# Performance work log

Measured on AMD Instinct MI355X. Metric: run time of the kernel, lower is better.

The kernel has to match this reference:

```python
import jax, jax.numpy as jnp
import numpy as np

EMBED_DIM = 256
N_LEVELS = 4
N_HEADS = 8
N_POINTS = 4
HEAD_DIM = EMBED_DIM // N_HEADS
N_QUERIES = 8192
BATCH = 2
LEVEL_SHAPES = np.array([[128, 128], [64, 64], [32, 32], [16, 16]], dtype=np.int32)
HMAX, WMAX = 128, 128
EPS = 1e-5


def setup_inputs() -> dict:
    key = jax.random.key(0)
    ks = jax.random.split(key, 10)
    scale = 1.0 / np.sqrt(EMBED_DIM)
    query = jax.random.normal(ks[0], (N_QUERIES, EMBED_DIM), jnp.float32)
    xy_reference_points = jax.random.uniform(ks[1], (N_QUERIES, 2), jnp.float32, 0.05, 0.95)
    val = jax.random.normal(ks[2], (BATCH, HMAX, WMAX, N_LEVELS, EMBED_DIM), jnp.float32)
    # zero outside each level's valid support (mimics sparse COO: absent entries read as 0)
    hh = jnp.arange(HMAX)[:, None, None]
    ww = jnp.arange(WMAX)[None, :, None]
    lh = jnp.asarray(LEVEL_SHAPES[:, 0])[None, None, :]
    lw = jnp.asarray(LEVEL_SHAPES[:, 1])[None, None, :]
    mask = ((hh < lh) & (ww < lw)).astype(jnp.float32)
    stacked_value_tensors = val * mask[None, :, :, :, None]
    return {
        "query": query,
        "xy_reference_points": xy_reference_points,
        "stacked_value_tensors": stacked_value_tensors,
        "W_off": (jax.random.normal(ks[3], (EMBED_DIM, N_LEVELS * N_POINTS * N_HEADS * 2)) * scale * 0.1).astype(jnp.float32),
        "b_off": (jax.random.normal(ks[4], (N_LEVELS * N_POINTS * N_HEADS * 2,)) * 0.5).astype(jnp.float32),
        "W_attn": (jax.random.normal(ks[5], (EMBED_DIM, N_LEVELS * N_POINTS * N_HEADS)) * scale).astype(jnp.float32),
        "b_attn": jnp.zeros((N_LEVELS * N_POINTS * N_HEADS,), jnp.float32),
        "W_out": (jax.random.normal(ks[6], (EMBED_DIM, EMBED_DIM)) * scale).astype(jnp.float32),
        "b_out": jnp.zeros((EMBED_DIM,), jnp.float32),
        "batch_offsets": jnp.array([0, N_QUERIES // 2], jnp.int32),
        "spatial_shapes": jnp.asarray(LEVEL_SHAPES, jnp.int32),
    }


def reference(query, xy_reference_points, stacked_value_tensors, W_off, b_off,
              W_attn, b_attn, W_out, b_out, batch_offsets, spatial_shapes):
    Q = query.shape[0]
    # sampling offsets & attention weights (torch Linear with W stored [in,out])
    off = (query @ W_off + b_off).reshape(Q, N_LEVELS, N_POINTS, N_HEADS, 2)
    aw = (query @ W_attn + b_attn).reshape(Q, N_LEVELS * N_POINTS, N_HEADS)
    aw = jax.nn.softmax(aw, axis=1).reshape(Q, N_LEVELS, N_POINTS, N_HEADS)
    # sampling locations: sigmoid(inverse_sigmoid(ref) + offsets), then map (0,1)->(-1,1)
    r = jnp.clip(xy_reference_points, 0.0, 1.0)
    inv = jnp.log(jnp.clip(r, EPS, 1.0) / jnp.clip(1.0 - r, EPS, 1.0))
    loc = jax.nn.sigmoid(inv[:, None, None, None, :] + off) * 2.0 - 1.0  # (Q,L,P,H,2)
    # per-query batch index from batch_offsets (start index per batch element)
    bidx = jnp.searchsorted(batch_offsets, jnp.arange(Q), side="right") - 1  # (Q,)
    b = bidx[:, None, None, None]
    h_sz = spatial_shapes[:, 0].astype(loc.dtype)[None, :, None, None]
    w_sz = spatial_shapes[:, 1].astype(loc.dtype)[None, :, None, None]
    x = ((loc[..., 0] + 1.0) * w_sz - 1.0) / 2.0  # (Q,L,P,H)
    y = ((loc[..., 1] + 1.0) * h_sz - 1.0) / 2.0
    x0 = jnp.floor(x).astype(jnp.int32); x1 = x0 + 1
    y0 = jnp.floor(y).astype(jnp.int32); y1 = y0 + 1
    wcap = (spatial_shapes[:, 1] - 1).astype(jnp.int32)[None, :, None, None]
    hcap = (spatial_shapes[:, 0] - 1).astype(jnp.int32)[None, :, None, None]
    x0 = jnp.clip(x0, 0, wcap); x1 = jnp.clip(x1, 0, wcap)
    y0 = jnp.clip(y0, 0, hcap); y1 = jnp.clip(y1, 0, hcap)
    x0f = x0.astype(x.dtype); x1f = x1.astype(x.dtype)
    y0f = y0.astype(y.dtype); y1f = y1.astype(y.dtype)
    wa = (x1f - x) * (y1f - y)  # pairs with (x0,y0), as in source
    wb = (x1f - x) * (y - y0f)  # (x0,y1)
    wc = (x - x0f) * (y1f - y)  # (x1,y0)
    wd = (x - x0f) * (y - y0f)  # (x1,y1)
    V = stacked_value_tensors.reshape(BATCH, HMAX, WMAX, N_LEVELS, N_HEADS, HEAD_DIM)
    l = jnp.arange(N_LEVELS)[None, :, None, None]
    h = jnp.arange(N_HEADS)[None, None, None, :]
    # NOTE: source indexes (batch, x, y, level, head) -> x indexes the height dim; levels are square
    def g(xi, yi):
        return V[b, xi, yi, l, h]  # (Q,L,P,H,HEAD_DIM)
    sampled = (wa[..., None] * g(x0, y0) + wb[..., None] * g(x0, y1)
               + wc[..., None] * g(x1, y0) + wd[..., None] * g(x1, y1))
    out = jnp.einsum("qlphd,qlph->qhd", sampled, aw).reshape(Q, EMBED_DIM)
    return out @ W_out + b_out
```

## Files before the change

kernel.cpp:

```cpp
#include <hip/hip_runtime.h>
#include <math.h>

#define ED      256
#define NL      4
#define NH      8
#define NP      4
#define HD      32
#define HMAX    128
#define WMAX    128
#define NLP     16
#define NC      128
#define NOFF_AW 384
#define QPB     4
#define NBK     1024
#define BSTRIDE (HMAX*WMAX*NL*ED)
#define XSTRIDE (WMAX*NL*ED)
#define YSTRIDE (NL*ED)
#define RPB     21760
#define PBC     (RPB*256)

typedef __attribute__((ext_vector_type(8))) __fp16   f16x8;
typedef __attribute__((ext_vector_type(4))) __fp16   f16x4;
typedef __attribute__((ext_vector_type(4))) float    f32x4;

__constant__ int LBASE_ROW[4] = {0, 16384, 20480, 21504};

__global__ __launch_bounds__(1024) void msda_prep_kernel(
    const float* __restrict__ V,
    const float* __restrict__ W_off,
    const float* __restrict__ W_attn,
    const float* __restrict__ W_out,
    const float* __restrict__ refp,
    const int*   __restrict__ batch_off,
    int n_batch,
    __fp16* __restrict__ Vc,
    __fp16* __restrict__ WcatT,
    __fp16* __restrict__ WoutT,
    int* __restrict__ bucket_of,
    int* __restrict__ perm,
    int nq, int nb, int nCompact, int nWconv)
{
    __shared__ int cnt[NBK];
    __shared__ int scan[NBK];
    const int bid = blockIdx.x;
    const int t   = threadIdx.x;

    if (bid < nCompact) {
        const int r    = bid * 16 + (t >> 6);
        const int lane = t & 63;
        const int e    = lane << 2;
        const int total_rows = nb * RPB;
        if (r < total_rows) {
            const int b  = r / RPB;
            const int rr = r - b * RPB;
            int l, base;
            if (rr < 16384)      { l = 0; base = 0; }
            else if (rr < 20480) { l = 1; base = 16384; }
            else if (rr < 21504) { l = 2; base = 20480; }
            else                 { l = 3; base = 21504; }
            const int pos = rr - base;
            const int lsh = 7 - l;
            const int xi  = pos >> lsh;
            const int yi  = pos & ((1 << lsh) - 1);
            const float4 src = *(const float4*)&V[(size_t)b * BSTRIDE +
                (size_t)xi * XSTRIDE + (size_t)yi * YSTRIDE + l * ED + e];
            f16x4 d;
            d[0] = (__fp16)src.x; d[1] = (__fp16)src.y;
            d[2] = (__fp16)src.z; d[3] = (__fp16)src.w;
            *(f16x4*)&Vc[(size_t)r * 256 + e] = d;
        }
    } else if (bid < nCompact + nWconv) {
        const int idx = (bid - nCompact) * 1024 + t;
        const int t2 = NOFF_AW * ED;
        const int t3 = ED * ED;
        if (idx < t2) {
            int c = idx >> 8, e = idx & 255;
            float v = (c < ED) ? W_off[e * ED + c] : W_attn[e * NC + (c - ED)];
            WcatT[idx] = (__fp16)v;
        } else if (idx < t2 + t3) {
            int i = idx - t2;
            int c = i >> 8, e = i & 255;
            WoutT[i] = (__fp16)W_out[e * ED + c];
        }
    } else {
        cnt[t] = 0;
        __syncthreads();
        const int iters = (nq + 1023) >> 10;
        for (int i = 0; i < iters; ++i) {
            int q = i * 1024 + t;
            if (q < nq) {
                int b = 0;
                for (int j = 1; j < n_batch; ++j)
                    if (batch_off[j] <= q) b = j;
                b = min(b, 3);
                float rx = refp[q * 2 + 0], ry = refp[q * 2 + 1];
                int bx = min(15, max(0, (int)(rx * 16.f)));
                int by = min(15, max(0, (int)(ry * 16.f)));
                int bk = (b << 8) | (by << 4) | bx;
                bucket_of[q] = bk;
                atomicAdd(&cnt[bk], 1);
            }
        }
        __syncthreads();
        scan[t] = cnt[t];
        __syncthreads();
        for (int d = 1; d < NBK; d <<= 1) {
            int v = scan[t];
            int u = (t >= d) ? scan[t - d] : 0;
            __syncthreads();
            scan[t] = v + u;
            __syncthreads();
        }
        cnt[t] = scan[t] - cnt[t];
        __syncthreads();
        for (int i = 0; i < iters; ++i) {
            int q = i * 1024 + t;
            if (q < nq) {
                int bk = bucket_of[q];
                int pos = atomicAdd(&cnt[bk], 1);
                perm[pos] = q;
            }
        }
    }
}

__global__ __launch_bounds__(256) void gemm_f16_kernel(
    const float*  __restrict__ A,
    const __fp16* __restrict__ BT,
    const float* __restrict__ bias0,
    const float* __restrict__ bias1,
    float* __restrict__ C,
    int M, int NTOT, int bias_split)
{
    const int wave = threadIdx.x >> 6;
    const int lane = threadIdx.x & 63;
    const int gw   = blockIdx.x * 4 + wave;
    const int ngroups = NTOT >> 6;
    const int mg = gw / ngroups, ng = gw % ngroups;
    const int m16 = mg * 16, n64 = ng * 64;
    if (m16 >= M) return;

    const int mrow = lane & 15;
    const int quad = lane >> 4;

    const float4* Arow = (const float4*)(A + (size_t)(m16 + mrow) * 256 + quad * 8);
    const f16x8* B0 = (const f16x8*)(BT + (size_t)(n64 +  0 + mrow) * 256 + quad * 8);
    const f16x8* B1 = (const f16x8*)(BT + (size_t)(n64 + 16 + mrow) * 256 + quad * 8);
    const f16x8* B2 = (const f16x8*)(BT + (size_t)(n64 + 32 + mrow) * 256 + quad * 8);
    const f16x8* B3 = (const f16x8*)(BT + (size_t)(n64 + 48 + mrow) * 256 + quad * 8);

    f32x4 acc0 = {0.f,0.f,0.f,0.f}, acc1 = acc0, acc2 = acc0, acc3 = acc0;
    #pragma unroll
    for (int kb = 0; kb < 8; ++kb) {
        float4 a0 = Arow[kb * 8 + 0];
        float4 a1 = Arow[kb * 8 + 1];
        float av[8] = {a0.x, a0.y, a0.z, a0.w, a1.x, a1.y, a1.z, a1.w};
        f16x8 ah, al;
        #pragma unroll
        for (int j = 0; j < 8; ++j) {
            __fp16 h = (__fp16)av[j];
            ah[j] = h;
            al[j] = (__fp16)(av[j] - (float)h);
        }
        f16x8 b0 = B0[kb * 4], b1 = B1[kb * 4], b2 = B2[kb * 4], b3 = B3[kb * 4];
        acc0 = __builtin_amdgcn_mfma_f32_16x16x32_f16(ah, b0, acc0, 0, 0, 0);
        acc1 = __builtin_amdgcn_mfma_f32_16x16x32_f16(ah, b1, acc1, 0, 0, 0);
        acc2 = __builtin_amdgcn_mfma_f32_16x16x32_f16(ah, b2, acc2, 0, 0, 0);
        acc3 = __builtin_amdgcn_mfma_f32_16x16x32_f16(ah, b3, acc3, 0, 0, 0);
        acc0 = __builtin_amdgcn_mfma_f32_16x16x32_f16(al, b0, acc0, 0, 0, 0);
        acc1 = __builtin_amdgcn_mfma_f32_16x16x32_f16(al, b1, acc1, 0, 0, 0);
        acc2 = __builtin_amdgcn_mfma_f32_16x16x32_f16(al, b2, acc2, 0, 0, 0);
        acc3 = __builtin_amdgcn_mfma_f32_16x16x32_f16(al, b3, acc3, 0, 0, 0);
    }

    const int col = lane & 15;
    f32x4 accs[4] = {acc0, acc1, acc2, acc3};
    #pragma unroll
    for (int i = 0; i < 4; ++i) {
        int n = n64 + i * 16 + col;
        float b = (n < bias_split) ? bias0[n] : bias1[n - bias_split];
        #pragma unroll
        for (int r = 0; r < 4; ++r) {
            int row = m16 + quad * 4 + r;
            C[(size_t)row * NTOT + n] = accs[i][r] + b;
        }
    }
}

__global__ __launch_bounds__(256) void gemm_ff16_kernel(
    const __fp16* __restrict__ A,
    const __fp16* __restrict__ BT,
    const float* __restrict__ bias,
    float* __restrict__ C,
    int M, int NTOT)
{
    const int wave = threadIdx.x >> 6;
    const int lane = threadIdx.x & 63;
    const int gw   = blockIdx.x * 4 + wave;
    const int ngroups = NTOT >> 6;
    const int mg = gw / ngroups, ng = gw % ngroups;
    const int m16 = mg * 16, n64 = ng * 64;
    if (m16 >= M) return;

    const int mrow = lane & 15;
    const int quad = lane >> 4;

    const f16x8* Arow = (const f16x8*)(A + (size_t)(m16 + mrow) * 256 + quad * 8);
    const f16x8* B0 = (const f16x8*)(BT + (size_t)(n64 +  0 + mrow) * 256 + quad * 8);
    const f16x8* B1 = (const f16x8*)(BT + (size_t)(n64 + 16 + mrow) * 256 + quad * 8);
    const f16x8* B2 = (const f16x8*)(BT + (size_t)(n64 + 32 + mrow) * 256 + quad * 8);
    const f16x8* B3 = (const f16x8*)(BT + (size_t)(n64 + 48 + mrow) * 256 + quad * 8);

    f32x4 acc0 = {0.f,0.f,0.f,0.f}, acc1 = acc0, acc2 = acc0, acc3 = acc0;
    #pragma unroll
    for (int kb = 0; kb < 8; ++kb) {
        f16x8 af = Arow[kb * 4];
        acc0 = __builtin_amdgcn_mfma_f32_16x16x32_f16(af, B0[kb * 4], acc0, 0, 0, 0);
        acc1 = __builtin_amdgcn_mfma_f32_16x16x32_f16(af, B1[kb * 4], acc1, 0, 0, 0);
        acc2 = __builtin_amdgcn_mfma_f32_16x16x32_f16(af, B2[kb * 4], acc2, 0, 0, 0);
        acc3 = __builtin_amdgcn_mfma_f32_16x16x32_f16(af, B3[kb * 4], acc3, 0, 0, 0);
    }

    const int col = lane & 15;
    f32x4 accs[4] = {acc0, acc1, acc2, acc3};
    #pragma unroll
    for (int i = 0; i < 4; ++i) {
        int n = n64 + i * 16 + col;
        float b = bias[n];
        #pragma unroll
        for (int r = 0; r < 4; ++r) {
            int row = m16 + quad * 4 + r;
            C[(size_t)row * NTOT + n] = accs[i][r] + b;
        }
    }
}

__global__ __launch_bounds__(256) void msda_sample_kernel(
    const float*  __restrict__ refp,
    const __fp16* __restrict__ Vc,
    const float*  __restrict__ off_aw,
    const int*    __restrict__ perm,
    const int*    __restrict__ batch_off,
    int n_batch,
    __fp16* __restrict__ out_pre,
    int q_total)
{
    __shared__ int    sqid[QPB];
    __shared__ float  law[QPB][NC];
    __shared__ float2 sminv[QPB][NH];
    __shared__ float2 sref[QPB];
    __shared__ int4   soff[QPB][NC];
    __shared__ float4 swt[QPB][NC];

    const int t = threadIdx.x;
    const int chunk = gridDim.x >> 3;
    const int pblk  = (blockIdx.x & 7) * chunk + (blockIdx.x >> 3);
    const int q0 = pblk * QPB;

    if (t < QPB) sqid[t] = perm[q0 + t];
    __syncthreads();

    {
        const int s = t >> 6, c = t & 63;
        const float* row = off_aw + (size_t)sqid[s] * NOFF_AW + ED;
        law[s][c]      = row[c];
        law[s][c + 64] = row[c + 64];
    }
    __syncthreads();

    if (t < QPB * NH) {
        const int s = t >> 3, h = t & 7;
        float m = -1e30f;
        #pragma unroll
        for (int lp = 0; lp < NLP; ++lp) m = fmaxf(m, law[s][lp * NH + h]);
        float sum = 0.f;
        #pragma unroll
        for (int lp = 0; lp < NLP; ++lp) sum += __expf(law[s][lp * NH + h] - m);
        sminv[s][h] = make_float2(m, 1.f / sum);
    } else if (t < QPB * NH + QPB) {
        const int s = t - QPB * NH;
        const int qid = sqid[s];
        float rx = refp[qid * 2 + 0], ry = refp[qid * 2 + 1];
        rx = fminf(fmaxf(rx, 0.f), 1.f);
        ry = fminf(fmaxf(ry, 0.f), 1.f);
        float ivx = __logf(fmaxf(rx, 1e-5f) / fmaxf(1.f - rx, 1e-5f));
        float ivy = __logf(fmaxf(ry, 1e-5f) / fmaxf(1.f - ry, 1e-5f));
        sref[s] = make_float2(ivx, ivy);
    }
    __syncthreads();

    {
        const int s = t >> 6;
        const int qid = sqid[s];
        int b = 0;
        for (int i = 1; i < n_batch; ++i)
            if (batch_off[i] <= qid) b = i;
        const int cb = b * PBC;
        const float2 iv = sref[s];
        const float* offrow = off_aw + (size_t)qid * NOFF_AW;

        #pragma unroll
        for (int half = 0; half < 2; ++half) {
            const int c = (t & 63) + half * 64;
            const int l = c >> 5;
            const int h = c & 7;
            const int lsh = 7 - l;
            const int sz  = 1 << lsh;
            const int cap = sz - 1;

            const float2 mi = sminv[s][h];
            const float a = __expf(law[s][c] - mi.x) * mi.y;

            const float ox = offrow[c * 2 + 0], oy = offrow[c * 2 + 1];
            float lx = 2.f / (1.f + __expf(-(iv.x + ox))) - 1.f;
            float ly = 2.f / (1.f + __expf(-(iv.y + oy))) - 1.f;
            float x = ((lx + 1.f) * (float)sz - 1.f) * 0.5f;
            float y = ((ly + 1.f) * (float)sz - 1.f) * 0.5f;
            int x0 = (int)floorf(x), y0 = (int)floorf(y);
            int x1 = x0 + 1, y1 = y0 + 1;
            x0 = min(max(x0, 0), cap); x1 = min(max(x1, 0), cap);
            y0 = min(max(y0, 0), cap); y1 = min(max(y1, 0), cap);
            float x0f = (float)x0, x1f = (float)x1;
            float y0f = (float)y0, y1f = (float)y1;

            float4 w;
            w.x = a * (x1f - x) * (y1f - y);
            w.y = a * (x1f - x) * (y - y0f);
            w.z = a * (x - x0f) * (y1f - y);
            w.w = a * (x - x0f) * (y - y0f);
            swt[s][c] = w;
            const int lb = cb + (LBASE_ROW[l] << 8);
            int4 o;
            o.x = lb + (((x0 << lsh) + y0) << 8);
            o.y = lb + (((x0 << lsh) + y1) << 8);
            o.z = lb + (((x1 << lsh) + y0) << 8);
            o.w = lb + (((x1 << lsh) + y1) << 8);
            soff[s][c] = o;
        }
    }
    __syncthreads();

    {
        const int s    = t >> 6;
        const int lane = t & 63;
        const int h    = lane >> 3;
        const int d4   = (lane & 7) << 2;
        const int inner = h * HD + d4;
        float4 acc = {0.f, 0.f, 0.f, 0.f};
        #pragma unroll 4
        for (int lp = 0; lp < NLP; ++lp) {
            const int c = lp * NH + h;
            int4   o = soff[s][c];
            float4 w = swt[s][c];
            f16x4 v0 = *(const f16x4*)&Vc[o.x + inner];
            f16x4 v1 = *(const f16x4*)&Vc[o.y + inner];
            f16x4 v2 = *(const f16x4*)&Vc[o.z + inner];
            f16x4 v3 = *(const f16x4*)&Vc[o.w + inner];
            acc.x += w.x*(float)v0[0] + w.y*(float)v1[0] + w.z*(float)v2[0] + w.w*(float)v3[0];
            acc.y += w.x*(float)v0[1] + w.y*(float)v1[1] + w.z*(float)v2[1] + w.w*(float)v3[1];
            acc.z += w.x*(float)v0[2] + w.y*(float)v1[2] + w.z*(float)v2[2] + w.w*(float)v3[2];
            acc.w += w.x*(float)v0[3] + w.y*(float)v1[3] + w.z*(float)v2[3] + w.w*(float)v3[3];
        }
        f16x4 o4;
        o4[0] = (__fp16)acc.x; o4[1] = (__fp16)acc.y;
        o4[2] = (__fp16)acc.z; o4[3] = (__fp16)acc.w;
        *(f16x4*)&out_pre[(size_t)sqid[s] * ED + inner] = o4;
    }
}

extern "C" void kernel_launch(void* const* d_in, const int* in_sizes, int n_in,
                              void* d_out, int out_size, void* d_ws, size_t ws_size,
                              hipStream_t stream) {
    const float* query  = (const float*)d_in[0];
    const float* refp   = (const float*)d_in[1];
    const float* V      = (const float*)d_in[2];
    const float* W_off  = (const float*)d_in[3];
    const float* b_off  = (const float*)d_in[4];
    const float* W_attn = (const float*)d_in[5];
    const float* b_attn = (const float*)d_in[6];
    const float* W_out  = (const float*)d_in[7];
    const float* b_out  = (const float*)d_in[8];
    const int*   boff   = (const int*)d_in[9];
    const int*   spat   = (const int*)d_in[10];
    const int n_batch   = in_sizes[9];
    const int nq        = in_sizes[0] / ED;
    const int nb        = in_sizes[2] / BSTRIDE;
    float* out = (float*)d_out;

    char* ws = (char*)d_ws;
    float*   off_aw    = (float*)ws;
    int*     perm      = (int*)(off_aw + (size_t)nq * NOFF_AW);
    int*     bucket_of = perm + nq;
    __fp16*  WcatT     = (__fp16*)(bucket_of + nq);
    __fp16*  WoutT     = WcatT + NOFF_AW * ED;
    __fp16*  out_pre   = WoutT + ED * ED;
    __fp16*  Vc        = out_pre + (size_t)nq * ED;

    {
        int nCompact = (nb * RPB + 15) / 16;
        int nWconv   = (NOFF_AW * ED + ED * ED + 1023) / 1024;
        msda_prep_kernel<<<nCompact + nWconv + 1, 1024, 0, stream>>>(
            V, W_off, W_attn, W_out, refp, boff, n_batch,
            Vc, WcatT, WoutT, bucket_of, perm, nq, nb, nCompact, nWconv);
    }
    {
        int waves = (nq / 16) * (NOFF_AW / 64);
        gemm_f16_kernel<<<(waves + 3) / 4, 256, 0, stream>>>(
            query, WcatT, b_off, b_attn, off_aw, nq, NOFF_AW, ED);
    }
    {
        msda_sample_kernel<<<nq / QPB, 256, 0, stream>>>(
            refp, Vc, off_aw, perm, boff, n_batch, out_pre, nq);
    }
    {
        int waves = (nq / 16) * (ED / 64);
        gemm_ff16_kernel<<<(waves + 3) / 4, 256, 0, stream>>>(
            out_pre, WoutT, b_out, out, nq, ED);
    }
}
```

Measured before the change: 266.4 us.

## Replace per-query gather with tile-binned sampling through shared-memory patches

Drops the query bucket sort. A plan kernel now computes bilinear weights per sample and scatters compact records into per-tile bins of each level using block-local histograms and global cursors. A tile kernel loads a 9x9 value patch into LDS and serves all samples in that tile from it, and a reduce kernel then sums the per-level-point samples into out_pre. This aims to turn scattered global gathers into LDS reuse. The cost is two extra launches, a large record buffer and an intermediate sampled buffer round-trip, fp16-packed weights, and a slow overflow fallback path.

```diff
diff --git a/kernel.cpp b/kernel.cpp
--- a/kernel.cpp
+++ b/kernel.cpp
@@ -12,36 +12,37 @@
 #define NC      128
 #define NOFF_AW 384
 #define QPB     4
-#define NBK     1024
 #define BSTRIDE (HMAX*WMAX*NL*ED)
 #define XSTRIDE (WMAX*NL*ED)
 #define YSTRIDE (NL*ED)
 #define RPB     21760
-#define PBC     (RPB*256)
+#define TILES_PB 340
+#define RECPB   2097152
+#define MAXB    4
 
 typedef __attribute__((ext_vector_type(8))) __fp16   f16x8;
 typedef __attribute__((ext_vector_type(4))) __fp16   f16x4;
 typedef __attribute__((ext_vector_type(4))) float    f32x4;
 
 __constant__ int LBASE_ROW[4] = {0, 16384, 20480, 21504};
+__constant__ int TBASE[4]     = {0, 256, 320, 336};
+
+__device__ __forceinline__ unsigned pack2h(float a, float b) {
+    union { __fp16 h[2]; unsigned u; } u;
+    u.h[0] = (__fp16)a; u.h[1] = (__fp16)b; return u.u;
+}
 
 __global__ __launch_bounds__(1024) void msda_prep_kernel(
     const float* __restrict__ V,
     const float* __restrict__ W_off,
     const float* __restrict__ W_attn,
     const float* __restrict__ W_out,
-    const float* __restrict__ refp,
-    const int*   __restrict__ batch_off,
-    int n_batch,
     __fp16* __restrict__ Vc,
     __fp16* __restrict__ WcatT,
     __fp16* __restrict__ WoutT,
-    int* __restrict__ bucket_of,
-    int* __restrict__ perm,
-    int nq, int nb, int nCompact, int nWconv)
-{
-    __shared__ int cnt[NBK];
-    __shared__ int scan[NBK];
+    unsigned* __restrict__ cursor,
+    int nb, int nCompact, int nWconv)
+{
     const int bid = blockIdx.x;
     const int t   = threadIdx.x;
 
@@ -83,44 +84,7 @@
             WoutT[i] = (__fp16)W_out[e * ED + c];
         }
     } else {
-        cnt[t] = 0;
-        __syncthreads();
-        const int iters = (nq + 1023) >> 10;
-        for (int i = 0; i < iters; ++i) {
-            int q = i * 1024 + t;
-            if (q < nq) {
-                int b = 0;
-                for (int j = 1; j < n_batch; ++j)
-                    if (batch_off[j] <= q) b = j;
-                b = min(b, 3);
-                float rx = refp[q * 2 + 0], ry = refp[q * 2 + 1];
-                int bx = min(15, max(0, (int)(rx * 16.f)));
-                int by = min(15, max(0, (int)(ry * 16.f)));
-                int bk = (b << 8) | (by << 4) | bx;
-                bucket_of[q] = bk;
-                atomicAdd(&cnt[bk], 1);
-            }
-        }
-        __syncthreads();
-        scan[t] = cnt[t];
-        __syncthreads();
-        for (int d = 1; d < NBK; d <<= 1) {
-            int v = scan[t];
-            int u = (t >= d) ? scan[t - d] : 0;
-            __syncthreads();
-            scan[t] = v + u;
-            __syncthreads();
-        }
-        cnt[t] = scan[t] - cnt[t];
-        __syncthreads();
-        for (int i = 0; i < iters; ++i) {
-            int q = i * 1024 + t;
-            if (q < nq) {
-                int bk = bucket_of[q];
-                int pos = atomicAdd(&cnt[bk], 1);
-                perm[pos] = q;
-            }
-        }
+        for (int i = t; i < TILES_PB * nb; i += 1024) cursor[i] = 0u;
     }
 }
 
@@ -235,34 +199,31 @@
     }
 }
 
-__global__ __launch_bounds__(256) void msda_sample_kernel(
+__global__ __launch_bounds__(256) void msda_plan_kernel(
     const float*  __restrict__ refp,
     const __fp16* __restrict__ Vc,
     const float*  __restrict__ off_aw,
-    const int*    __restrict__ perm,
     const int*    __restrict__ batch_off,
-    int n_batch,
-    __fp16* __restrict__ out_pre,
-    int q_total)
-{
-    __shared__ int    sqid[QPB];
-    __shared__ float  law[QPB][NC];
-    __shared__ float2 sminv[QPB][NH];
-    __shared__ float2 sref[QPB];
-    __shared__ int4   soff[QPB][NC];
-    __shared__ float4 swt[QPB][NC];
-
-    const int t = threadIdx.x;
-    const int chunk = gridDim.x >> 3;
-    const int pblk  = (blockIdx.x & 7) * chunk + (blockIdx.x >> 3);
-    const int q0 = pblk * QPB;
-
-    if (t < QPB) sqid[t] = perm[q0 + t];
-    __syncthreads();
+    int n_batch, int nb,
+    unsigned* __restrict__ cursor,
+    int4*     __restrict__ recB,
+    __fp16*   __restrict__ sampled,
+    int nq)
+{
+    __shared__ float    law[QPB][NC];
+    __shared__ float2   sminv[QPB][NH];
+    __shared__ float2   sref[QPB];
+    __shared__ unsigned hist[TILES_PB * MAXB];
+
+    const int t  = threadIdx.x;
+    const int q0 = blockIdx.x * QPB;
+    const int tiles_total = TILES_PB * nb;
+
+    for (int i = t; i < TILES_PB * MAXB; i += 256) hist[i] = 0u;
 
     {
         const int s = t >> 6, c = t & 63;
-        const float* row = off_aw + (size_t)sqid[s] * NOFF_AW + ED;
+        const float* row = off_aw + (size_t)(q0 + s) * NOFF_AW + ED;
         law[s][c]      = row[c];
         law[s][c + 64] = row[c + 64];
     }
@@ -279,7 +240,7 @@
         sminv[s][h] = make_float2(m, 1.f / sum);
     } else if (t < QPB * NH + QPB) {
         const int s = t - QPB * NH;
-        const int qid = sqid[s];
+        const int qid = q0 + s;
         float rx = refp[qid * 2 + 0], ry = refp[qid * 2 + 1];
         rx = fminf(fmaxf(rx, 0.f), 1.f);
         ry = fminf(fmaxf(ry, 0.f), 1.f);
@@ -289,83 +250,192 @@
     }
     __syncthreads();
 
-    {
-        const int s = t >> 6;
-        const int qid = sqid[s];
-        int b = 0;
-        for (int i = 1; i < n_batch; ++i)
-            if (batch_off[i] <= qid) b = i;
-        const int cb = b * PBC;
-        const float2 iv = sref[s];
-        const float* offrow = off_aw + (size_t)qid * NOFF_AW;
-
-        #pragma unroll
-        for (int half = 0; half < 2; ++half) {
-            const int c = (t & 63) + half * 64;
-            const int l = c >> 5;
+    const int s = t >> 6;
+    const int qid = q0 + s;
+    int b = 0;
+    for (int i = 1; i < n_batch; ++i)
+        if (batch_off[i] <= qid) b = i;
+    const float2 iv = sref[s];
+    const float* offrow = off_aw + (size_t)qid * NOFF_AW;
+
+    int4   rec[2];
+    int    tileg[2];
+    float4 wf[2];
+    int    gx0[2], gy0[2], gx1[2], gy1[2];
+
+    #pragma unroll
+    for (int half = 0; half < 2; ++half) {
+        const int c = (t & 63) + half * 64;
+        const int l = c >> 5;
+        const int h = c & 7;
+        const int lsh = 7 - l;
+        const int sz  = 1 << lsh;
+        const int cap = sz - 1;
+
+        const float2 mi = sminv[s][h];
+        const float a = __expf(law[s][c] - mi.x) * mi.y;
+
+        const float ox = offrow[c * 2 + 0], oy = offrow[c * 2 + 1];
+        float lx = 2.f / (1.f + __expf(-(iv.x + ox))) - 1.f;
+        float ly = 2.f / (1.f + __expf(-(iv.y + oy))) - 1.f;
+        float x = ((lx + 1.f) * (float)sz - 1.f) * 0.5f;
+        float y = ((ly + 1.f) * (float)sz - 1.f) * 0.5f;
+        int x0 = (int)floorf(x), y0 = (int)floorf(y);
+        int x1 = x0 + 1, y1 = y0 + 1;
+        x0 = min(max(x0, 0), cap); x1 = min(max(x1, 0), cap);
+        y0 = min(max(y0, 0), cap); y1 = min(max(y1, 0), cap);
+        float x0f = (float)x0, x1f = (float)x1;
+        float y0f = (float)y0, y1f = (float)y1;
+
+        float4 w;
+        w.x = a * (x1f - x) * (y1f - y);
+        w.y = a * (x1f - x) * (y - y0f);
+        w.z = a * (x - x0f) * (y1f - y);
+        w.w = a * (x - x0f) * (y - y0f);
+
+        const int ntr = sz >> 3;
+        const int tx = x0 >> 3, ty = y0 >> 3;
+        const int til = b * TILES_PB + TBASE[l] + tx * ntr + ty;
+        tileg[half] = til;
+        wf[half] = w;
+        gx0[half] = x0; gy0[half] = y0; gx1[half] = x1; gy1[half] = y1;
+        rec[half].x = (qid << 7) | c;
+        rec[half].y = (x0 - (tx << 3)) | ((y0 - (ty << 3)) << 4) |
+                      ((x1 - (tx << 3)) << 8) | ((y1 - (ty << 3)) << 12);
+        rec[half].z = (int)pack2h(w.x, w.y);
+        rec[half].w = (int)pack2h(w.z, w.w);
+        atomicAdd(&hist[til], 1u);
+    }
+    __syncthreads();
+
+    for (int i = t; i < tiles_total; i += 256) {
+        unsigned cloc = hist[i];
+        hist[i] = (cloc > 0u) ? atomicAdd(&cursor[i], cloc) : 0u;
+    }
+    __syncthreads();
+
+    #pragma unroll
+    for (int half = 0; half < 2; ++half) {
+        const int til = tileg[half];
+        const unsigned pos = atomicAdd(&hist[til], 1u);
+        const int c = rec[half].x & 127;
+        const int l = c >> 5;
+        const unsigned capl = 2048u << (2 * l);
+        if (pos < capl) {
+            const int b2  = til / TILES_PB;
+            const int tin = til - b2 * TILES_PB - TBASE[l];
+            recB[(size_t)b2 * RECPB + (size_t)l * 524288 +
+                 (size_t)tin * capl + pos] = rec[half];
+        } else {
             const int h = c & 7;
-            const int lsh = 7 - l;
-            const int sz  = 1 << lsh;
-            const int cap = sz - 1;
-
-            const float2 mi = sminv[s][h];
-            const float a = __expf(law[s][c] - mi.x) * mi.y;
-
-            const float ox = offrow[c * 2 + 0], oy = offrow[c * 2 + 1];
-            float lx = 2.f / (1.f + __expf(-(iv.x + ox))) - 1.f;
-            float ly = 2.f / (1.f + __expf(-(iv.y + oy))) - 1.f;
-            float x = ((lx + 1.f) * (float)sz - 1.f) * 0.5f;
-            float y = ((ly + 1.f) * (float)sz - 1.f) * 0.5f;
-            int x0 = (int)floorf(x), y0 = (int)floorf(y);
-            int x1 = x0 + 1, y1 = y0 + 1;
-            x0 = min(max(x0, 0), cap); x1 = min(max(x1, 0), cap);
-            y0 = min(max(y0, 0), cap); y1 = min(max(y1, 0), cap);
-            float x0f = (float)x0, x1f = (float)x1;
-            float y0f = (float)y0, y1f = (float)y1;
-
-            float4 w;
-            w.x = a * (x1f - x) * (y1f - y);
-            w.y = a * (x1f - x) * (y - y0f);
-            w.z = a * (x - x0f) * (y1f - y);
-            w.w = a * (x - x0f) * (y - y0f);
-            swt[s][c] = w;
-            const int lb = cb + (LBASE_ROW[l] << 8);
-            int4 o;
-            o.x = lb + (((x0 << lsh) + y0) << 8);
-            o.y = lb + (((x0 << lsh) + y1) << 8);
-            o.z = lb + (((x1 << lsh) + y0) << 8);
-            o.w = lb + (((x1 << lsh) + y1) << 8);
-            soff[s][c] = o;
+            const int lsh = 7 - l, sz = 1 << lsh;
+            const int rowb = b * RPB + LBASE_ROW[l];
+            const int dest = rec[half].x;
+            const float4 w = wf[half];
+            const __fp16* p00 = Vc + ((size_t)(rowb + gx0[half]*sz + gy0[half]))*256 + h*HD;
+            const __fp16* p01 = Vc + ((size_t)(rowb + gx0[half]*sz + gy1[half]))*256 + h*HD;
+            const __fp16* p10 = Vc + ((size_t)(rowb + gx1[half]*sz + gy0[half]))*256 + h*HD;
+            const __fp16* p11 = Vc + ((size_t)(rowb + gx1[half]*sz + gy1[half]))*256 + h*HD;
+            for (int d = 0; d < HD; ++d) {
+                float v = w.x*(float)p00[d] + w.y*(float)p01[d]
+                        + w.z*(float)p10[d] + w.w*(float)p11[d];
+                sampled[(size_t)dest * HD + d] = (__fp16)v;
+            }
+        }
+    }
+}
+
+__global__ __launch_bounds__(256) void msda_tile_kernel(
+    const __fp16*   __restrict__ Vc,
+    const unsigned* __restrict__ cursor,
+    const int4*     __restrict__ recB,
+    __fp16*         __restrict__ sampled)
+{
+    __shared__ __fp16 patch[81 * 264];
+
+    const int bid = blockIdx.x;
+    const int b   = bid >> 10;
+    const int sid = bid & 1023;
+    const int l   = sid >> 8;
+    const int s2  = sid & 255;
+    const int sbits = 2 * l;
+    const int tin   = s2 >> sbits;
+    const int slice = s2 & ((1 << sbits) - 1);
+    const int lsh = 7 - l, sz = 1 << lsh, ntr = sz >> 3, cap = sz - 1;
+    const int tx = tin / ntr, ty = tin - tx * ntr;
+    const int x0b = tx << 3, y0b = ty << 3;
+    const int rowb = b * RPB + LBASE_ROW[l];
+
+    const int wv = threadIdx.x >> 6, lane = threadIdx.x & 63;
+
+    for (int r = wv; r < 81; r += 4) {
+        const int xi = r / 9, yi = r - xi * 9;
+        const int gx = x0b + xi, gy = y0b + yi;
+        if (gx <= cap && gy <= cap) {
+            f16x4 v = *(const f16x4*)&Vc[((size_t)(rowb + gx * sz + gy)) * 256 + lane * 4];
+            *(f16x4*)&patch[r * 264 + lane * 4] = v;
         }
     }
     __syncthreads();
 
-    {
-        const int s    = t >> 6;
-        const int lane = t & 63;
-        const int h    = lane >> 3;
-        const int d4   = (lane & 7) << 2;
-        const int inner = h * HD + d4;
-        float4 acc = {0.f, 0.f, 0.f, 0.f};
-        #pragma unroll 4
-        for (int lp = 0; lp < NLP; ++lp) {
-            const int c = lp * NH + h;
-            int4   o = soff[s][c];
-            float4 w = swt[s][c];
-            f16x4 v0 = *(const f16x4*)&Vc[o.x + inner];
-            f16x4 v1 = *(const f16x4*)&Vc[o.y + inner];
-            f16x4 v2 = *(const f16x4*)&Vc[o.z + inner];
-            f16x4 v3 = *(const f16x4*)&Vc[o.w + inner];
-            acc.x += w.x*(float)v0[0] + w.y*(float)v1[0] + w.z*(float)v2[0] + w.w*(float)v3[0];
-            acc.y += w.x*(float)v0[1] + w.y*(float)v1[1] + w.z*(float)v2[1] + w.w*(float)v3[1];
-            acc.z += w.x*(float)v0[2] + w.y*(float)v1[2] + w.z*(float)v2[2] + w.w*(float)v3[2];
-            acc.w += w.x*(float)v0[3] + w.y*(float)v1[3] + w.z*(float)v2[3] + w.w*(float)v3[3];
-        }
-        f16x4 o4;
-        o4[0] = (__fp16)acc.x; o4[1] = (__fp16)acc.y;
-        o4[2] = (__fp16)acc.z; o4[3] = (__fp16)acc.w;
-        *(f16x4*)&out_pre[(size_t)sqid[s] * ED + inner] = o4;
-    }
+    const int tglob = b * TILES_PB + TBASE[l] + tin;
+    unsigned cnt = cursor[tglob];
+    const unsigned capl = 2048u << sbits;
+    if (cnt > capl) cnt = capl;
+    const int nsl = 1 << sbits;
+    const unsigned per = (cnt + (unsigned)nsl - 1u) >> sbits;
+    const unsigned lo = (unsigned)slice * per;
+    unsigned hi = lo + per; if (hi > cnt) hi = cnt;
+
+    const int4* recT = recB + (size_t)b * RECPB + (size_t)l * 524288 +
+                       (size_t)tin * capl;
+    const int g = lane >> 3, j = lane & 7;
+
+    for (unsigned base = lo + (unsigned)wv * 8u; base < hi; base += 32u) {
+        const unsigned idx = base + (unsigned)g;
+        if (idx < hi) {
+            int4 rec = recT[idx];
+            const int dest = rec.x;
+            const int db = (dest & 7) * HD + j * 4;
+            const int lx0 = rec.y & 15, ly0 = (rec.y >> 4) & 15;
+            const int lx1 = (rec.y >> 8) & 15, ly1 = (rec.y >> 12) & 15;
+            union { unsigned u; __fp16 h[2]; } pA, pB;
+            pA.u = (unsigned)rec.z; pB.u = (unsigned)rec.w;
+            const float w0 = (float)pA.h[0], w1 = (float)pA.h[1];
+            const float w2 = (float)pB.h[0], w3 = (float)pB.h[1];
+            f16x4 p00 = *(f16x4*)&patch[(lx0 * 9 + ly0) * 264 + db];
+            f16x4 p01 = *(f16x4*)&patch[(lx0 * 9 + ly1) * 264 + db];
+            f16x4 p10 = *(f16x4*)&patch[(lx1 * 9 + ly0) * 264 + db];
+            f16x4 p11 = *(f16x4*)&patch[(lx1 * 9 + ly1) * 264 + db];
+            f16x4 o;
+            #pragma unroll
+            for (int k = 0; k < 4; ++k)
+                o[k] = (__fp16)(w0*(float)p00[k] + w1*(float)p01[k] +
+                                w2*(float)p10[k] + w3*(float)p11[k]);
+            *(f16x4*)&sampled[(size_t)dest * HD + j * 4] = o;
+        }
+    }
+}
+
+__global__ __launch_bounds__(256) void msda_reduce_kernel(
+    const __fp16* __restrict__ sampled,
+    __fp16* __restrict__ out_pre)
+{
+    const int t = threadIdx.x;
+    const int grp = t >> 3, j = t & 7;
+    const int gid = blockIdx.x * 32 + grp;
+    const int q = gid >> 3, h = gid & 7;
+    float acc0 = 0.f, acc1 = 0.f, acc2 = 0.f, acc3 = 0.f;
+    #pragma unroll
+    for (int lp = 0; lp < NLP; ++lp) {
+        f16x4 v = *(const f16x4*)&sampled[((size_t)(q * 128 + lp * 8 + h)) * HD + j * 4];
+        acc0 += (float)v[0]; acc1 += (float)v[1];
+        acc2 += (float)v[2]; acc3 += (float)v[3];
+    }
+    f16x4 o;
+    o[0] = (__fp16)acc0; o[1] = (__fp16)acc1;
+    o[2] = (__fp16)acc2; o[3] = (__fp16)acc3;
+    *(f16x4*)&out_pre[(size_t)q * ED + h * HD + j * 4] = o;
 }
 
 extern "C" void kernel_launch(void* const* d_in, const int* in_sizes, int n_in,
@@ -381,37 +451,39 @@
     const float* W_out  = (const float*)d_in[7];
     const float* b_out  = (const float*)d_in[8];
     const int*   boff   = (const int*)d_in[9];
-    const int*   spat   = (const int*)d_in[10];
     const int n_batch   = in_sizes[9];
     const int nq        = in_sizes[0] / ED;
     const int nb        = in_sizes[2] / BSTRIDE;
     float* out = (float*)d_out;
 
     char* ws = (char*)d_ws;
-    float*   off_aw    = (float*)ws;
-    int*     perm      = (int*)(off_aw + (size_t)nq * NOFF_AW);
-    int*     bucket_of = perm + nq;
-    __fp16*  WcatT     = (__fp16*)(bucket_of + nq);
-    __fp16*  WoutT     = WcatT + NOFF_AW * ED;
-    __fp16*  out_pre   = WoutT + ED * ED;
-    __fp16*  Vc        = out_pre + (size_t)nq * ED;
+    float*    off_aw  = (float*)ws;
+    __fp16*   WcatT   = (__fp16*)(off_aw + (size_t)nq * NOFF_AW);
+    __fp16*   WoutT   = WcatT + NOFF_AW * ED;
+    __fp16*   out_pre = WoutT + ED * ED;
+    __fp16*   Vc      = out_pre + (size_t)nq * ED;
+    unsigned* cursor  = (unsigned*)(Vc + (size_t)nb * RPB * 256);
+    char*     aligned = (char*)(cursor + TILES_PB * MAXB);
+    aligned = (char*)(((size_t)aligned + 15) & ~(size_t)15);
+    int4*     recB    = (int4*)aligned;
+    __fp16*   sampled = (__fp16*)(recB + (size_t)nb * RECPB);
 
     {
         int nCompact = (nb * RPB + 15) / 16;
         int nWconv   = (NOFF_AW * ED + ED * ED + 1023) / 1024;
         msda_prep_kernel<<<nCompact + nWconv + 1, 1024, 0, stream>>>(
-            V, W_off, W_attn, W_out, refp, boff, n_batch,
-            Vc, WcatT, WoutT, bucket_of, perm, nq, nb, nCompact, nWconv);
+            V, W_off, W_attn, W_out, Vc, WcatT, WoutT, cursor,
+            nb, nCompact, nWconv);
     }
     {
         int waves = (nq / 16) * (NOFF_AW / 64);
         gemm_f16_kernel<<<(waves + 3) / 4, 256, 0, stream>>>(
             query, WcatT, b_off, b_attn, off_aw, nq, NOFF_AW, ED);
     }
-    {
-        msda_sample_kernel<<<nq / QPB, 256, 0, stream>>>(
-            refp, Vc, off_aw, perm, boff, n_batch, out_pre, nq);
-    }
+    msda_plan_kernel<<<nq / QPB, 256, 0, stream>>>(
+        refp, Vc, off_aw, boff, n_batch, nb, cursor, recB, sampled, nq);
+    msda_tile_kernel<<<nb * 1024, 256, 0, stream>>>(Vc, cursor, recB, sampled);
+    msda_reduce_kernel<<<nq / 4, 256, 0, stream>>>(sampled, out_pre);
     {
         int waves = (nq / 16) * (ED / 64);
         gemm_ff16_kernel<<<(waves + 3) / 4, 256, 0, stream>>>(
```

Result: slower. 338.5 us (+27.1%).

## Store compacted values head-planar so neighbouring y-taps are one contiguous load

Applied to the files above, without the earlier changes.

The fp16 value compaction now writes a per-level, per-head planar layout [level][head][x][y][32]. In that layout the (x,y0) and (x,y1) bilinear taps sit next to each other in memory. The sampling kernel therefore keeps two offsets per sample instead of four, issues two 16-byte loads per lane, and combines the y0 and y1 halves with a lane shuffle. Clamped edges where y1 equals y0 are handled by folding the weights together. This reduces gather instruction count and scattered memory transactions, at the cost of strided 64-byte stores in the prep kernel and an extra cross-lane reduction.

```diff
diff --git a/kernel.cpp b/kernel.cpp
--- a/kernel.cpp
+++ b/kernel.cpp
@@ -48,7 +48,8 @@
     if (bid < nCompact) {
         const int r    = bid * 16 + (t >> 6);
         const int lane = t & 63;
-        const int e    = lane << 2;
+        const int h    = lane >> 3;
+        const int j4   = lane & 7;
         const int total_rows = nb * RPB;
         if (r < total_rows) {
             const int b  = r / RPB;
@@ -62,12 +63,16 @@
             const int lsh = 7 - l;
             const int xi  = pos >> lsh;
             const int yi  = pos & ((1 << lsh) - 1);
+            const int plane32 = (1 << (2 * lsh)) * 32;
             const float4 src = *(const float4*)&V[(size_t)b * BSTRIDE +
-                (size_t)xi * XSTRIDE + (size_t)yi * YSTRIDE + l * ED + e];
+                (size_t)xi * XSTRIDE + (size_t)yi * YSTRIDE + l * ED +
+                h * HD + j4 * 4];
             f16x4 d;
             d[0] = (__fp16)src.x; d[1] = (__fp16)src.y;
             d[2] = (__fp16)src.z; d[3] = (__fp16)src.w;
-            *(f16x4*)&Vc[(size_t)r * 256 + e] = d;
+            const size_t dst = (size_t)b * PBC + (size_t)LBASE_ROW[l] * 256 +
+                               (size_t)h * plane32 + (size_t)pos * 32 + j4 * 4;
+            *(f16x4*)&Vc[dst] = d;
         }
     } else if (bid < nCompact + nWconv) {
         const int idx = (bid - nCompact) * 1024 + t;
@@ -249,7 +254,7 @@
     __shared__ float  law[QPB][NC];
     __shared__ float2 sminv[QPB][NH];
     __shared__ float2 sref[QPB];
-    __shared__ int4   soff[QPB][NC];
+    __shared__ int2   soff[QPB][NC];
     __shared__ float4 swt[QPB][NC];
 
     const int t = threadIdx.x;
@@ -303,10 +308,11 @@
         for (int half = 0; half < 2; ++half) {
             const int c = (t & 63) + half * 64;
             const int l = c >> 5;
-            const int h = c & 7;
             const int lsh = 7 - l;
             const int sz  = 1 << lsh;
             const int cap = sz - 1;
+            const int h = c & 7;
+            const int plane32 = (sz * sz) << 5;
 
             const float2 mi = sminv[s][h];
             const float a = __expf(law[s][c] - mi.x) * mi.y;
@@ -323,18 +329,19 @@
             float x0f = (float)x0, x1f = (float)x1;
             float y0f = (float)y0, y1f = (float)y1;
 
-            float4 w;
-            w.x = a * (x1f - x) * (y1f - y);
-            w.y = a * (x1f - x) * (y - y0f);
-            w.z = a * (x - x0f) * (y1f - y);
-            w.w = a * (x - x0f) * (y - y0f);
-            swt[s][c] = w;
-            const int lb = cb + (LBASE_ROW[l] << 8);
-            int4 o;
-            o.x = lb + (((x0 << lsh) + y0) << 8);
-            o.y = lb + (((x0 << lsh) + y1) << 8);
-            o.z = lb + (((x1 << lsh) + y0) << 8);
-            o.w = lb + (((x1 << lsh) + y1) << 8);
+            float w00 = a * (x1f - x) * (y1f - y);
+            float w01 = a * (x1f - x) * (y - y0f);
+            float w10 = a * (x - x0f) * (y1f - y);
+            float w11 = a * (x - x0f) * (y - y0f);
+            if (y1 == y0) {
+                w00 += w01; w01 = 0.f;
+                w10 += w11; w11 = 0.f;
+            }
+            swt[s][c] = make_float4(w00, w01, w10, w11);
+            const int lb = cb + (LBASE_ROW[l] << 8) + h * plane32;
+            int2 o;
+            o.x = lb + (((x0 << lsh) + y0) << 5);
+            o.y = lb + (((x1 << lsh) + y0) << 5);
             soff[s][c] = o;
         }
     }
@@ -344,27 +351,37 @@
         const int s    = t >> 6;
         const int lane = t & 63;
         const int h    = lane >> 3;
-        const int d4   = (lane & 7) << 2;
-        const int inner = h * HD + d4;
-        float4 acc = {0.f, 0.f, 0.f, 0.f};
+        const int j    = lane & 7;
+        const int top  = j >> 2;
+        const int blk  = j & 3;
+
+        float acc[8];
+        #pragma unroll
+        for (int k = 0; k < 8; ++k) acc[k] = 0.f;
+
         #pragma unroll 4
         for (int lp = 0; lp < NLP; ++lp) {
             const int c = lp * NH + h;
-            int4   o = soff[s][c];
+            int2   o = soff[s][c];
             float4 w = swt[s][c];
-            f16x4 v0 = *(const f16x4*)&Vc[o.x + inner];
-            f16x4 v1 = *(const f16x4*)&Vc[o.y + inner];
-            f16x4 v2 = *(const f16x4*)&Vc[o.z + inner];
-            f16x4 v3 = *(const f16x4*)&Vc[o.w + inner];
-            acc.x += w.x*(float)v0[0] + w.y*(float)v1[0] + w.z*(float)v2[0] + w.w*(float)v3[0];
-            acc.y += w.x*(float)v0[1] + w.y*(float)v1[1] + w.z*(float)v2[1] + w.w*(float)v3[1];
-            acc.z += w.x*(float)v0[2] + w.y*(float)v1[2] + w.z*(float)v2[2] + w.w*(float)v3[2];
-            acc.w += w.x*(float)v0[3] + w.y*(float)v1[3] + w.z*(float)v2[3] + w.w*(float)v3[3];
-        }
-        f16x4 o4;
-        o4[0] = (__fp16)acc.x; o4[1] = (__fp16)acc.y;
-        o4[2] = (__fp16)acc.z; o4[3] = (__fp16)acc.w;
-        *(f16x4*)&out_pre[(size_t)sqid[s] * ED + inner] = o4;
+            f16x8 va = *(const f16x8*)&Vc[o.x + j * 8];
+            f16x8 vb = *(const f16x8*)&Vc[o.y + j * 8];
+            const float wa = top ? w.y : w.x;
+            const float wb = top ? w.w : w.z;
+            #pragma unroll
+            for (int k = 0; k < 8; ++k)
+                acc[k] += wa * (float)va[k] + wb * (float)vb[k];
+        }
+        #pragma unroll
+        for (int k = 0; k < 8; ++k)
+            acc[k] += __shfl_xor(acc[k], 4);
+
+        if (top == 0) {
+            f16x8 o8;
+            #pragma unroll
+            for (int k = 0; k < 8; ++k) o8[k] = (__fp16)acc[k];
+            *(f16x8*)&out_pre[(size_t)sqid[s] * ED + h * HD + blk * 8] = o8;
+        }
     }
 }
 
@@ -381,7 +398,6 @@
     const float* W_out  = (const float*)d_in[7];
     const float* b_out  = (const float*)d_in[8];
     const int*   boff   = (const int*)d_in[9];
-    const int*   spat   = (const int*)d_in[10];
     const int n_batch   = in_sizes[9];
     const int nq        = in_sizes[0] / ED;
     const int nb        = in_sizes[2] / BSTRIDE;
```

New measurement: 265.1 us. About the same (-0.5%).
